# Optimization experiments

Measured on AMD Instinct MI355X. Metric: run time of the kernel, lower is better.

The kernel has to match this reference:

```python
import jax, jax.numpy as jnp
import numpy as np

B, N, C, H = 2, 2048, 768, 12
DH = C // H
SCALE = DH ** (-0.5)


def setup_inputs() -> dict:
    key = jax.random.key(0)
    k1, k2, k3, k4 = jax.random.split(key, 4)
    x = jax.random.normal(k1, (B, N, 1, C), dtype=jnp.float32)
    mask = jax.random.randint(k2, (B, N), 0, 2) > 0  # bool keep-mask
    w_qkv = jax.random.normal(k3, (3 * C, C), dtype=jnp.float32) * (C ** -0.5)
    w_proj = jax.random.normal(k4, (C, C), dtype=jnp.float32) * (C ** -0.5)
    b_proj = jnp.zeros((C,), dtype=jnp.float32)
    return {"x": x, "mask": mask, "w_qkv": w_qkv, "w_proj": w_proj, "b_proj": b_proj}


def reference(x, mask, w_qkv, w_proj, b_proj):
    Bs, N1, N2, Cs = x.shape  # N2 == 1 required by the original reshape
    # qkv: Linear(dim, 3*dim, bias=False) -> reshape (B,N1,3,H,Dh) -> (3,B,H,N1,Dh)
    qkv = jnp.einsum('bnoc,dc->bnod', x, w_qkv)  # (B,N1,1,3C)
    qkv = qkv.reshape(Bs, N1, 3, H, Cs // H).transpose(2, 0, 3, 1, 4)
    q, k, v = qkv[0], qkv[1], qkv[2]  # each (B,H,N,Dh)
    attn = jnp.einsum('bhid,bhjd->bhij', q, k) * SCALE  # (B,H,N,N)
    mask_value = -jnp.finfo(attn.dtype).max
    pair = mask[:, None, :] & mask[:, :, None]  # (B,N,N), broadcast over heads
    attn = jnp.where(pair[:, None, :, :], attn, mask_value)
    attn = jax.nn.softmax(attn, axis=-1)
    # dropout in eval mode -> identity
    out = jnp.einsum('bhij,bhjd->bhid', attn, v)  # (B,H,N,Dh)
    out = out.transpose(0, 2, 1, 3).reshape(Bs, N1, Cs)  # (B,N,C)
    out = out @ w_proj.T + b_proj
    return out
```

## Files before the change

kernel.cpp:

```cpp
#include <hip/hip_runtime.h>

#define NN 2048
#define CC 768
#define HH 12
#define SCALE2 0.18033688011112042f
#define NEGB  -3.0e35f
#define THR   12.0f

typedef __attribute__((ext_vector_type(4))) float f32x4;
typedef __attribute__((ext_vector_type(8))) short short8;
typedef __attribute__((ext_vector_type(8))) unsigned short u16x8;

#if __has_builtin(__builtin_amdgcn_exp2f)
#define EXP2(x) __builtin_amdgcn_exp2f(x)
#else
#define EXP2(x) exp2f(x)
#endif

static __device__ __forceinline__ unsigned short f2bf(float f) {
    unsigned u = __float_as_uint(f);
    u += 0x7FFFu + ((u >> 16) & 1u);
    return (unsigned short)(u >> 16);
}

static __device__ __forceinline__ f32x4 MFMA(u16x8 a, u16x8 b, f32x4 c) {
    union { u16x8 u; short8 s; } ua, ub;
    ua.u = a; ub.u = b;
    return __builtin_amdgcn_mfma_f32_16x16x32_bf16(ua.s, ub.s, c, 0, 0, 0);
}

static __device__ __forceinline__ void glds16(const void* g, void* l) {
    __builtin_amdgcn_global_load_lds(
        (const __attribute__((address_space(1))) unsigned int*)g,
        (__attribute__((address_space(3))) unsigned int*)l, 16, 0, 0);
}

__global__ void cvt_f32_bf16(const float* __restrict__ in,
                             unsigned short* __restrict__ out, int n8) {
    int i = blockIdx.x * blockDim.x + threadIdx.x;
    if (i >= n8) return;
    const f32x4* p = (const f32x4*)(in + (size_t)i * 8);
    f32x4 a = p[0], b = p[1];
    u16x8 o;
    o[0] = f2bf(a[0]); o[1] = f2bf(a[1]); o[2] = f2bf(a[2]); o[3] = f2bf(a[3]);
    o[4] = f2bf(b[0]); o[5] = f2bf(b[1]); o[6] = f2bf(b[2]); o[7] = f2bf(b[3]);
    *(u16x8*)(out + (size_t)i * 8) = o;
}

__launch_bounds__(256)
__global__ void gemm_bt(const unsigned short* __restrict__ A,
                        const unsigned short* __restrict__ Bt,
                        unsigned short* __restrict__ outB,
                        float* __restrict__ outF,
                        const float* __restrict__ bias,
                        int M, int N, int K, int qcols) {
    __shared__ __align__(16) unsigned short As[128][64];
    __shared__ __align__(16) unsigned short Bs[128][64];
    int tid = threadIdx.x, lane = tid & 63, w = tid >> 6;
    int wm = w >> 1, wn = w & 1;
    int li = lane & 15, g = lane >> 4;
    int bn = blockIdx.x, bm = blockIdx.y;

    f32x4 acc[4][4] = {};

    int lrow = lane >> 3, lsl = lane & 7;
    int xcol = (lsl ^ (lrow & 7)) * 8;
    const unsigned short* Ag = A  + (size_t)(bm * 128 + w * 32 + lrow) * K + xcol;
    const unsigned short* Bg = Bt + (size_t)(bn * 128 + w * 32 + lrow) * K + xcol;

    for (int k0 = 0; k0 < K; k0 += 64) {
        __syncthreads();
#pragma unroll
        for (int i = 0; i < 4; ++i) {
            glds16(Ag + (size_t)(i * 8) * K + k0, &As[w * 32 + i * 8][0]);
            glds16(Bg + (size_t)(i * 8) * K + k0, &Bs[w * 32 + i * 8][0]);
        }
        __syncthreads();
#pragma unroll
        for (int kk = 0; kk < 2; ++kk) {
            u16x8 af[4], bf[4];
#pragma unroll
            for (int mi = 0; mi < 4; ++mi)
                af[mi] = *(const u16x8*)&As[wm * 64 + mi * 16 + li][((4 * kk + g) ^ (li & 7)) * 8];
#pragma unroll
            for (int ni = 0; ni < 4; ++ni)
                bf[ni] = *(const u16x8*)&Bs[wn * 64 + ni * 16 + li][((4 * kk + g) ^ (li & 7)) * 8];
            __builtin_amdgcn_s_setprio(1);
#pragma unroll
            for (int mi = 0; mi < 4; ++mi)
#pragma unroll
                for (int ni = 0; ni < 4; ++ni)
                    acc[mi][ni] = MFMA(af[mi], bf[ni], acc[mi][ni]);
            __builtin_amdgcn_s_setprio(0);
        }
    }

#pragma unroll
    for (int mi = 0; mi < 4; ++mi) {
#pragma unroll
        for (int ni = 0; ni < 4; ++ni) {
#pragma unroll
            for (int r = 0; r < 4; ++r) {
                int row = bm * 128 + wm * 64 + mi * 16 + g * 4 + r;
                int col = bn * 128 + wn * 64 + ni * 16 + li;
                float v = acc[mi][ni][r];
                if (outB) {
                    if (col < qcols) v *= SCALE2;
                    outB[(size_t)row * N + col] = f2bf(v);
                } else {
                    outF[(size_t)row * N + col] = v + bias[col];
                }
            }
        }
    }
}

__launch_bounds__(128, 2)
__global__ void attn_kernel(const unsigned short* __restrict__ qkv,
                            const int* __restrict__ mask,
                            unsigned short* __restrict__ hout) {
    __shared__ __align__(16) unsigned short Ks[2][64][64];
    __shared__ __align__(16) unsigned int   Vp[2][64][32];
    __shared__ __align__(16) float pen[NN];

    int tid = threadIdx.x;
    int lane = tid & 63;
    int w = tid >> 6;
    int li = lane & 15, g = lane >> 4;

    int lb = (blockIdx.x & 7) * 96 + (blockIdx.x >> 3);
    int qb = lb & 31;
    int bh = lb >> 5;
    int b = bh / HH, head = bh % HH;
    const int* mb = mask + b * NN;

    {
        int i = tid * 16;
#pragma unroll
        for (int s = 0; s < 4; ++s) {
            union { int4 v; int a[4]; } m4;
            m4.v = *(const int4*)&mb[i + s * 4];
            f32x4 p;
#pragma unroll
            for (int r = 0; r < 4; ++r) p[r] = m4.a[r] ? 0.f : NEGB;
            *(f32x4*)&pen[i + s * 4] = p;
        }
    }

    const unsigned short* qbase = qkv + (size_t)(b * NN) * 2304;

    u16x8 qf[2][2];
    float pm[2];
#pragma unroll
    for (int qt = 0; qt < 2; ++qt) {
        int qrow = qb * 64 + w * 32 + qt * 16 + li;
        const unsigned short* qp = qbase + (size_t)qrow * 2304 + head * 64;
        u16x8 a0 = *(const u16x8*)(qp + g * 8);
        u16x8 a1 = *(const u16x8*)(qp + 32 + g * 8);
        bool rk = mb[qrow] != 0;
        pm[qt] = rk ? 1.f : 0.f;
        if (!rk) { a0 = (u16x8)0; a1 = (u16x8)0; }
        qf[qt][0] = a0; qf[qt][1] = a1;
    }

    int xslot = ((lane & 7) ^ ((lane >> 3) & 7)) * 8;
    const unsigned short* kg = qbase + CC + head * 64 + xslot
                               + (size_t)(w * 32 + (lane >> 3)) * 2304;

    int m2 = tid >> 3;
    int vkc = (tid & 7) * 8;
    int ma = m2 * 2, mbp = ma + 1;
    int vca = (ma & 16) | ((ma & 6) << 1) | ((ma & 8) >> 2) | (ma & 1);
    int vcb = (mbp & 16) | ((mbp & 6) << 1) | ((mbp & 8) >> 2) | (mbp & 1);
    const unsigned short* vg = qbase + 2 * CC + head * 64 + vkc;

    u16x8 vr0, vr1, vr2, vr3;
    auto stageK = [&](int buf, int kb) {
#pragma unroll
        for (int s = 0; s < 4; ++s)
            glds16(kg + (size_t)(kb + s * 8) * 2304, &Ks[buf][w * 32 + s * 8][0]);
    };
    auto loadV = [&](int kb) {
        vr0 = *(const u16x8*)(vg + (size_t)(kb + 4 * m2) * 2304);
        vr1 = *(const u16x8*)(vg + (size_t)(kb + 4 * m2 + 1) * 2304);
        vr2 = *(const u16x8*)(vg + (size_t)(kb + 4 * m2 + 2) * 2304);
        vr3 = *(const u16x8*)(vg + (size_t)(kb + 4 * m2 + 3) * 2304);
    };
    auto writeV = [&](int buf) {
        union { u16x8 v; unsigned u[4]; } a0, a1, a2, a3;
        a0.v = vr0; a1.v = vr1; a2.v = vr2; a3.v = vr3;
        unsigned* vp = &Vp[buf][0][0];
#pragma unroll
        for (int e = 0; e < 8; ++e) {
            int dd = (e + (tid & 7)) & 7;
            int d0 = vkc + dd;
            unsigned dwa = __builtin_amdgcn_perm(a1.u[dd >> 1], a0.u[dd >> 1],
                                                 (dd & 1) ? 0x07060302u : 0x05040100u);
            unsigned dwb = __builtin_amdgcn_perm(a3.u[dd >> 1], a2.u[dd >> 1],
                                                 (dd & 1) ? 0x07060302u : 0x05040100u);
            vp[d0 * 32 + (((vca >> 2) ^ (d0 & 7)) << 2) + (vca & 3)] = dwa;
            vp[d0 * 32 + (((vcb >> 2) ^ (d0 & 7)) << 2) + (vcb & 3)] = dwb;
        }
    };

    stageK(0, 0);
    loadV(0);
    writeV(0);
    loadV(64);

    float m_st[2] = {-1e30f, -1e30f};
    float l_st[2] = {0.f, 0.f};
    f32x4 acc[2][4] = {};

    for (int it = 0; it < 32; ++it) {
        __syncthreads();
        int cur = it & 1, nx = cur ^ 1;
        if (it < 31) { writeV(nx); stageK(nx, (it + 1) * 64); }
        if (it < 30) loadV((it + 2) * 64);

        f32x4 st[2][4];
        __builtin_amdgcn_s_setprio(1);
#pragma unroll
        for (int t = 0; t < 4; ++t) {
            const unsigned short* kr = &Ks[cur][t * 16 + li][0];
            u16x8 k0 = *(const u16x8*)(kr + ((g ^ (li & 7)) * 8));
            u16x8 k1 = *(const u16x8*)(kr + (((4 + g) ^ (li & 7)) * 8));
            f32x4 z0 = {}, z1 = {};
            z0 = MFMA(k0, qf[0][0], z0);
            z1 = MFMA(k0, qf[1][0], z1);
            z0 = MFMA(k1, qf[0][1], z0);
            z1 = MFMA(k1, qf[1][1], z1);
            st[0][t] = z0; st[1][t] = z1;
        }
        __builtin_amdgcn_s_setprio(0);

        const float* pp = &pen[it * 64];
        f32x4 p4[4];
#pragma unroll
        for (int t = 0; t < 4; ++t) p4[t] = *(const f32x4*)&pp[t * 16 + g * 4];
        float lmax[2] = {-3e38f, -3e38f};
#pragma unroll
        for (int qt = 0; qt < 2; ++qt)
#pragma unroll
            for (int t = 0; t < 4; ++t) {
                st[qt][t] += p4[t] * pm[qt];
                lmax[qt] = fmaxf(lmax[qt], fmaxf(fmaxf(st[qt][t][0], st[qt][t][1]),
                                                 fmaxf(st[qt][t][2], st[qt][t][3])));
            }
        bool trig = (lmax[0] > m_st[0] + THR) || (lmax[1] > m_st[1] + THR);
        if (__any(trig)) {
#pragma unroll
            for (int qt = 0; qt < 2; ++qt) {
                float tm = lmax[qt];
                tm = fmaxf(tm, __shfl_xor(tm, 16));
                tm = fmaxf(tm, __shfl_xor(tm, 32));
                float mnew = fmaxf(m_st[qt], tm);
                float alpha = EXP2(m_st[qt] - mnew);
                float ar[4];
#pragma unroll
                for (int r = 0; r < 4; ++r) ar[r] = __shfl(alpha, g * 4 + r);
#pragma unroll
                for (int dt = 0; dt < 4; ++dt)
#pragma unroll
                    for (int r = 0; r < 4; ++r) acc[qt][dt][r] *= ar[r];
                l_st[qt] *= alpha;
                m_st[qt] = mnew;
            }
        }
        union { unsigned u[8]; u16x8 v[2]; } pu[2];
#pragma unroll
        for (int qt = 0; qt < 2; ++qt) {
            float lsum = 0.f;
#pragma unroll
            for (int t = 0; t < 4; ++t) {
                f32x4 e4;
#pragma unroll
                for (int r = 0; r < 4; ++r) { e4[r] = EXP2(st[qt][t][r] - m_st[qt]); lsum += e4[r]; }
                pu[qt].u[t * 2]     = __builtin_amdgcn_perm(__float_as_uint(e4[1]),
                                                            __float_as_uint(e4[0]), 0x07060302u);
                pu[qt].u[t * 2 + 1] = __builtin_amdgcn_perm(__float_as_uint(e4[3]),
                                                            __float_as_uint(e4[2]), 0x07060302u);
            }
            lsum += __shfl_xor(lsum, 16);
            lsum += __shfl_xor(lsum, 32);
            l_st[qt] += lsum;
        }

        __builtin_amdgcn_s_setprio(1);
#pragma unroll
        for (int h = 0; h < 2; ++h)
#pragma unroll
            for (int dt = 0; dt < 4; ++dt) {
                const unsigned* vr = &Vp[cur][dt * 16 + li][0];
                u16x8 vf = *(const u16x8*)(vr + (((4 * h + g) ^ (li & 7)) << 2));
                acc[0][dt] = MFMA(pu[0].v[h], vf, acc[0][dt]);
                acc[1][dt] = MFMA(pu[1].v[h], vf, acc[1][dt]);
            }
        __builtin_amdgcn_s_setprio(0);
    }

#pragma unroll
    for (int qt = 0; qt < 2; ++qt) {
        float linv = 1.0f / l_st[qt];
        float lr[4];
#pragma unroll
        for (int r = 0; r < 4; ++r) lr[r] = __shfl(linv, g * 4 + r);
        size_t obase = ((size_t)(b * NN + qb * 64 + w * 32 + qt * 16)) * CC + head * 64;
#pragma unroll
        for (int dt = 0; dt < 4; ++dt)
#pragma unroll
            for (int r = 0; r < 4; ++r)
                hout[obase + (size_t)(g * 4 + r) * CC + dt * 16 + li] =
                    f2bf(acc[qt][dt][r] * lr[r]);
    }
}

extern "C" void kernel_launch(void* const* d_in, const int* in_sizes, int n_in,
                              void* d_out, int out_size, void* d_ws, size_t ws_size,
                              hipStream_t stream) {
    const float* x     = (const float*)d_in[0];
    const int*   mask  = (const int*)d_in[1];
    const float* wqkv  = (const float*)d_in[2];
    const float* wproj = (const float*)d_in[3];
    const float* bproj = (const float*)d_in[4];
    float* out = (float*)d_out;

    unsigned short* x_bf     = (unsigned short*)d_ws;
    unsigned short* wqkv_bf  = x_bf + 3145728;
    unsigned short* wproj_bf = wqkv_bf + 1769472;
    unsigned short* qkv_bf   = wproj_bf + 589824;
    unsigned short* h_bf     = qkv_bf + 9437184;

    cvt_f32_bf16<<<1536, 256, 0, stream>>>(x, x_bf, 393216);
    cvt_f32_bf16<<<864, 256, 0, stream>>>(wqkv, wqkv_bf, 221184);
    cvt_f32_bf16<<<288, 256, 0, stream>>>(wproj, wproj_bf, 73728);

    gemm_bt<<<dim3(18, 32), 256, 0, stream>>>(x_bf, wqkv_bf, qkv_bf, nullptr,
                                              nullptr, 4096, 2304, 768, 768);
    attn_kernel<<<768, 128, 0, stream>>>(qkv_bf, mask, h_bf);
    gemm_bt<<<dim3(6, 32), 256, 0, stream>>>(h_bf, wproj_bf, nullptr, out,
                                             bproj, 4096, 768, 768, 0);
}
```

Measured before the change: 238.9 us.

## Split attention key blocks across wave pairs and merge partial softmax states

Doubles the attention block to four waves. Each pair of waves covers the same 32 query rows but takes a different half of each 64-key tile, so each wave runs half the QK and PV MFMAs per iteration. The mask penalty is now loaded as the initial accumulator of the QK MFMA instead of being added afterwards. At the end, the partial outputs and their max/sum statistics are merged through shared memory that reuses the K/V buffers. This raises the number of waves available to hide latency, at the cost of an extra merge pass, two more block barriers and per-wave max tracking that is not shared within a pair.

```diff
diff --git a/kernel.cpp b/kernel.cpp
--- a/kernel.cpp
+++ b/kernel.cpp
@@ -115,7 +115,7 @@
     }
 }
 
-__launch_bounds__(128, 2)
+__launch_bounds__(256, 3)
 __global__ void attn_kernel(const unsigned short* __restrict__ qkv,
                             const int* __restrict__ mask,
                             unsigned short* __restrict__ hout) {
@@ -127,6 +127,9 @@
     int lane = tid & 63;
     int w = tid >> 6;
     int li = lane & 15, g = lane >> 4;
+    int qh = w >> 1;
+    int jh = (w & 1) * 32;
+    int hh = w & 1;
 
     int lb = (blockIdx.x & 7) * 96 + (blockIdx.x >> 3);
     int qb = lb & 31;
@@ -135,16 +138,18 @@
     const int* mb = mask + b * NN;
 
     {
-        int i = tid * 16;
-#pragma unroll
-        for (int s = 0; s < 4; ++s) {
-            union { int4 v; int a[4]; } m4;
-            m4.v = *(const int4*)&mb[i + s * 4];
-            f32x4 p;
-#pragma unroll
-            for (int r = 0; r < 4; ++r) p[r] = m4.a[r] ? 0.f : NEGB;
-            *(f32x4*)&pen[i + s * 4] = p;
-        }
+        int i = tid * 8;
+        union { int4 v; int a[4]; } m0, m1;
+        m0.v = *(const int4*)&mb[i];
+        m1.v = *(const int4*)&mb[i + 4];
+        f32x4 p0, p1;
+#pragma unroll
+        for (int r = 0; r < 4; ++r) {
+            p0[r] = m0.a[r] ? 0.f : NEGB;
+            p1[r] = m1.a[r] ? 0.f : NEGB;
+        }
+        *(f32x4*)&pen[i] = p0;
+        *(f32x4*)&pen[i + 4] = p1;
     }
 
     const unsigned short* qbase = qkv + (size_t)(b * NN) * 2304;
@@ -153,7 +158,7 @@
     float pm[2];
 #pragma unroll
     for (int qt = 0; qt < 2; ++qt) {
-        int qrow = qb * 64 + w * 32 + qt * 16 + li;
+        int qrow = qb * 64 + qh * 32 + qt * 16 + li;
         const unsigned short* qp = qbase + (size_t)qrow * 2304 + head * 64;
         u16x8 a0 = *(const u16x8*)(qp + g * 8);
         u16x8 a1 = *(const u16x8*)(qp + 32 + g * 8);
@@ -165,41 +170,34 @@
 
     int xslot = ((lane & 7) ^ ((lane >> 3) & 7)) * 8;
     const unsigned short* kg = qbase + CC + head * 64 + xslot
-                               + (size_t)(w * 32 + (lane >> 3)) * 2304;
-
-    int m2 = tid >> 3;
+                               + (size_t)(w * 16 + (lane >> 3)) * 2304;
+
+    int vm = tid >> 3;
     int vkc = (tid & 7) * 8;
-    int ma = m2 * 2, mbp = ma + 1;
-    int vca = (ma & 16) | ((ma & 6) << 1) | ((ma & 8) >> 2) | (ma & 1);
-    int vcb = (mbp & 16) | ((mbp & 6) << 1) | ((mbp & 8) >> 2) | (mbp & 1);
+    int vcol = (vm & 16) | ((vm & 6) << 1) | ((vm & 8) >> 2) | (vm & 1);
+    int vslot = vcol >> 2, vsub = vcol & 3;
     const unsigned short* vg = qbase + 2 * CC + head * 64 + vkc;
 
-    u16x8 vr0, vr1, vr2, vr3;
+    u16x8 va, vb;
     auto stageK = [&](int buf, int kb) {
-#pragma unroll
-        for (int s = 0; s < 4; ++s)
-            glds16(kg + (size_t)(kb + s * 8) * 2304, &Ks[buf][w * 32 + s * 8][0]);
+        glds16(kg + (size_t)kb * 2304,       &Ks[buf][w * 16][0]);
+        glds16(kg + (size_t)(kb + 8) * 2304, &Ks[buf][w * 16 + 8][0]);
     };
     auto loadV = [&](int kb) {
-        vr0 = *(const u16x8*)(vg + (size_t)(kb + 4 * m2) * 2304);
-        vr1 = *(const u16x8*)(vg + (size_t)(kb + 4 * m2 + 1) * 2304);
-        vr2 = *(const u16x8*)(vg + (size_t)(kb + 4 * m2 + 2) * 2304);
-        vr3 = *(const u16x8*)(vg + (size_t)(kb + 4 * m2 + 3) * 2304);
+        va = *(const u16x8*)(vg + (size_t)(kb + 2 * vm) * 2304);
+        vb = *(const u16x8*)(vg + (size_t)(kb + 2 * vm + 1) * 2304);
     };
     auto writeV = [&](int buf) {
-        union { u16x8 v; unsigned u[4]; } a0, a1, a2, a3;
-        a0.v = vr0; a1.v = vr1; a2.v = vr2; a3.v = vr3;
+        union { u16x8 v; unsigned u[4]; } ua, ub;
+        ua.v = va; ub.v = vb;
         unsigned* vp = &Vp[buf][0][0];
 #pragma unroll
         for (int e = 0; e < 8; ++e) {
             int dd = (e + (tid & 7)) & 7;
+            unsigned dw = __builtin_amdgcn_perm(ub.u[dd >> 1], ua.u[dd >> 1],
+                                                (dd & 1) ? 0x07060302u : 0x05040100u);
             int d0 = vkc + dd;
-            unsigned dwa = __builtin_amdgcn_perm(a1.u[dd >> 1], a0.u[dd >> 1],
-                                                 (dd & 1) ? 0x07060302u : 0x05040100u);
-            unsigned dwb = __builtin_amdgcn_perm(a3.u[dd >> 1], a2.u[dd >> 1],
-                                                 (dd & 1) ? 0x07060302u : 0x05040100u);
-            vp[d0 * 32 + (((vca >> 2) ^ (d0 & 7)) << 2) + (vca & 3)] = dwa;
-            vp[d0 * 32 + (((vcb >> 2) ^ (d0 & 7)) << 2) + (vcb & 3)] = dwb;
+            vp[d0 * 32 + ((vslot ^ (d0 & 7)) << 2) + vsub] = dw;
         }
     };
 
@@ -209,7 +207,7 @@
     loadV(64);
 
     float m_st[2] = {-1e30f, -1e30f};
-    float l_st[2] = {0.f, 0.f};
+    float l_part[2] = {0.f, 0.f};
     f32x4 acc[2][4] = {};
 
     for (int it = 0; it < 32; ++it) {
@@ -218,14 +216,23 @@
         if (it < 31) { writeV(nx); stageK(nx, (it + 1) * 64); }
         if (it < 30) loadV((it + 2) * 64);
 
-        f32x4 st[2][4];
+        const float* pp = &pen[it * 64 + jh];
+        f32x4 ci[2][2];
+#pragma unroll
+        for (int t = 0; t < 2; ++t) {
+            f32x4 p4 = *(const f32x4*)&pp[t * 16 + g * 4];
+            ci[0][t] = p4 * pm[0];
+            ci[1][t] = p4 * pm[1];
+        }
+
+        f32x4 st[2][2];
         __builtin_amdgcn_s_setprio(1);
 #pragma unroll
-        for (int t = 0; t < 4; ++t) {
-            const unsigned short* kr = &Ks[cur][t * 16 + li][0];
+        for (int t = 0; t < 2; ++t) {
+            const unsigned short* kr = &Ks[cur][jh + t * 16 + li][0];
             u16x8 k0 = *(const u16x8*)(kr + ((g ^ (li & 7)) * 8));
             u16x8 k1 = *(const u16x8*)(kr + (((4 + g) ^ (li & 7)) * 8));
-            f32x4 z0 = {}, z1 = {};
+            f32x4 z0 = ci[0][t], z1 = ci[1][t];
             z0 = MFMA(k0, qf[0][0], z0);
             z1 = MFMA(k0, qf[1][0], z1);
             z0 = MFMA(k1, qf[0][1], z0);
@@ -234,19 +241,13 @@
         }
         __builtin_amdgcn_s_setprio(0);
 
-        const float* pp = &pen[it * 64];
-        f32x4 p4[4];
-#pragma unroll
-        for (int t = 0; t < 4; ++t) p4[t] = *(const f32x4*)&pp[t * 16 + g * 4];
-        float lmax[2] = {-3e38f, -3e38f};
-#pragma unroll
-        for (int qt = 0; qt < 2; ++qt)
-#pragma unroll
-            for (int t = 0; t < 4; ++t) {
-                st[qt][t] += p4[t] * pm[qt];
-                lmax[qt] = fmaxf(lmax[qt], fmaxf(fmaxf(st[qt][t][0], st[qt][t][1]),
-                                                 fmaxf(st[qt][t][2], st[qt][t][3])));
-            }
+        float lmax[2];
+#pragma unroll
+        for (int qt = 0; qt < 2; ++qt) {
+            f32x4 a = st[qt][0], c = st[qt][1];
+            lmax[qt] = fmaxf(fmaxf(fmaxf(a[0], a[1]), fmaxf(a[2], a[3])),
+                             fmaxf(fmaxf(c[0], c[1]), fmaxf(c[2], c[3])));
+        }
         bool trig = (lmax[0] > m_st[0] + THR) || (lmax[1] > m_st[1] + THR);
         if (__any(trig)) {
 #pragma unroll
@@ -263,55 +264,92 @@
                 for (int dt = 0; dt < 4; ++dt)
 #pragma unroll
                     for (int r = 0; r < 4; ++r) acc[qt][dt][r] *= ar[r];
-                l_st[qt] *= alpha;
+                l_part[qt] *= alpha;
                 m_st[qt] = mnew;
             }
         }
-        union { unsigned u[8]; u16x8 v[2]; } pu[2];
-#pragma unroll
-        for (int qt = 0; qt < 2; ++qt) {
-            float lsum = 0.f;
-#pragma unroll
-            for (int t = 0; t < 4; ++t) {
+        union { unsigned u[4]; u16x8 v8; } pu[2];
+#pragma unroll
+        for (int qt = 0; qt < 2; ++qt)
+#pragma unroll
+            for (int t = 0; t < 2; ++t) {
                 f32x4 e4;
 #pragma unroll
-                for (int r = 0; r < 4; ++r) { e4[r] = EXP2(st[qt][t][r] - m_st[qt]); lsum += e4[r]; }
+                for (int r = 0; r < 4; ++r) {
+                    e4[r] = EXP2(st[qt][t][r] - m_st[qt]);
+                    l_part[qt] += e4[r];
+                }
                 pu[qt].u[t * 2]     = __builtin_amdgcn_perm(__float_as_uint(e4[1]),
                                                             __float_as_uint(e4[0]), 0x07060302u);
                 pu[qt].u[t * 2 + 1] = __builtin_amdgcn_perm(__float_as_uint(e4[3]),
                                                             __float_as_uint(e4[2]), 0x07060302u);
             }
-            lsum += __shfl_xor(lsum, 16);
-            lsum += __shfl_xor(lsum, 32);
-            l_st[qt] += lsum;
-        }
 
         __builtin_amdgcn_s_setprio(1);
 #pragma unroll
-        for (int h = 0; h < 2; ++h)
-#pragma unroll
-            for (int dt = 0; dt < 4; ++dt) {
-                const unsigned* vr = &Vp[cur][dt * 16 + li][0];
-                u16x8 vf = *(const u16x8*)(vr + (((4 * h + g) ^ (li & 7)) << 2));
-                acc[0][dt] = MFMA(pu[0].v[h], vf, acc[0][dt]);
-                acc[1][dt] = MFMA(pu[1].v[h], vf, acc[1][dt]);
-            }
+        for (int dt = 0; dt < 4; ++dt) {
+            const unsigned* vr = &Vp[cur][dt * 16 + li][0];
+            u16x8 vf = *(const u16x8*)(vr + (((4 * hh + g) ^ (li & 7)) << 2));
+            acc[0][dt] = MFMA(pu[0].v8, vf, acc[0][dt]);
+            acc[1][dt] = MFMA(pu[1].v8, vf, acc[1][dt]);
+        }
         __builtin_amdgcn_s_setprio(0);
     }
 
+    float l_red[2];
 #pragma unroll
     for (int qt = 0; qt < 2; ++qt) {
-        float linv = 1.0f / l_st[qt];
-        float lr[4];
-#pragma unroll
-        for (int r = 0; r < 4; ++r) lr[r] = __shfl(linv, g * 4 + r);
-        size_t obase = ((size_t)(b * NN + qb * 64 + w * 32 + qt * 16)) * CC + head * 64;
-#pragma unroll
-        for (int dt = 0; dt < 4; ++dt)
-#pragma unroll
-            for (int r = 0; r < 4; ++r)
-                hout[obase + (size_t)(g * 4 + r) * CC + dt * 16 + li] =
-                    f2bf(acc[qt][dt][r] * lr[r]);
+        float l = l_part[qt];
+        l += __shfl_xor(l, 16);
+        l += __shfl_xor(l, 32);
+        l_red[qt] = l;
+    }
+
+    float* mrg = (float*)&Ks[0][0][0];
+    float* mlb = (float*)&Vp[0][0][0];
+    __syncthreads();
+    if (w & 1) {
+#pragma unroll
+        for (int qt = 0; qt < 2; ++qt) {
+#pragma unroll
+            for (int dt = 0; dt < 4; ++dt)
+#pragma unroll
+                for (int r = 0; r < 4; ++r)
+                    mrg[qh * 2048 + (qt * 16 + g * 4 + r) * 64 + dt * 16 + li] =
+                        acc[qt][dt][r];
+            if (g == 0) {
+                mlb[qh * 64 + qt * 16 + li] = m_st[qt];
+                mlb[qh * 64 + 32 + qt * 16 + li] = l_red[qt];
+            }
+        }
+    }
+    __syncthreads();
+    if (!(w & 1)) {
+#pragma unroll
+        for (int qt = 0; qt < 2; ++qt) {
+            float m_p = mlb[qh * 64 + qt * 16 + li];
+            float l_p = mlb[qh * 64 + 32 + qt * 16 + li];
+            float ms = fmaxf(m_st[qt], m_p);
+            float ae = EXP2(m_st[qt] - ms);
+            float ap = EXP2(m_p - ms);
+            float linv = 1.0f / (l_red[qt] * ae + l_p * ap);
+            float fe = ae * linv, fp = ap * linv;
+            float fer[4], fpr[4];
+#pragma unroll
+            for (int r = 0; r < 4; ++r) {
+                fer[r] = __shfl(fe, g * 4 + r);
+                fpr[r] = __shfl(fp, g * 4 + r);
+            }
+            size_t obase = ((size_t)(b * NN + qb * 64 + qh * 32 + qt * 16)) * CC + head * 64;
+#pragma unroll
+            for (int dt = 0; dt < 4; ++dt)
+#pragma unroll
+                for (int r = 0; r < 4; ++r) {
+                    float vpart = mrg[qh * 2048 + (qt * 16 + g * 4 + r) * 64 + dt * 16 + li];
+                    hout[obase + (size_t)(g * 4 + r) * CC + dt * 16 + li] =
+                        f2bf(acc[qt][dt][r] * fer[r] + vpart * fpr[r]);
+                }
+        }
     }
 }
 
@@ -337,7 +375,7 @@
 
     gemm_bt<<<dim3(18, 32), 256, 0, stream>>>(x_bf, wqkv_bf, qkv_bf, nullptr,
                                               nullptr, 4096, 2304, 768, 768);
-    attn_kernel<<<768, 128, 0, stream>>>(qkv_bf, mask, h_bf);
+    attn_kernel<<<768, 256, 0, stream>>>(qkv_bf, mask, h_bf);
     gemm_bt<<<dim3(6, 32), 256, 0, stream>>>(h_bf, wproj_bf, nullptr, out,
                                              bproj, 4096, 768, 768, 0);
 }
```

Measured after the change: 229.7 us. 3.8% less time.
